# Kernel tuning notes

Hardware: AMD Instinct MI355X
Metric: run time of the kernel (lower is better)

## Reference

```python
import jax, jax.numpy as jnp
import numpy as np

N_NODES = 65536
N_EDGES = 1048576
IN_DIM = 128
OUT_DIM = 64


def setup_inputs() -> dict:
    key = jax.random.key(0)
    k = jax.random.split(key, 7)
    stdv = 1.0 / np.sqrt(OUT_DIM)
    return {
        "input_feature": jax.random.normal(k[0], (N_NODES, IN_DIM), dtype=jnp.float32),
        "edge_row": jax.random.randint(k[1], (N_EDGES,), 0, N_NODES, dtype=jnp.int32),
        "edge_col": jax.random.randint(k[2], (N_EDGES,), 0, N_NODES, dtype=jnp.int32),
        "edge_vals": jax.random.uniform(k[3], (N_EDGES,), dtype=jnp.float32),
        "prior_probability_tensor": jax.random.uniform(k[4], (N_NODES, OUT_DIM), dtype=jnp.float32),
        "weight": jax.random.uniform(k[5], (IN_DIM, OUT_DIM), minval=-stdv, maxval=stdv, dtype=jnp.float32),
        "bias": jax.random.uniform(k[6], (OUT_DIM,), minval=-stdv, maxval=stdv, dtype=jnp.float32),
    }


def reference(input_feature, edge_row, edge_col, edge_vals, prior_probability_tensor, weight, bias):
    # support = X @ W  : [N, out_dim]
    support = input_feature @ weight
    # sparse spmm: out[i] = sum_e A[i, col(e)] * support[col(e)] over edges with row(e)==i
    msgs = edge_vals[:, None] * support[edge_col]          # [E, out_dim] gather
    output = jax.ops.segment_sum(msgs, edge_row, num_segments=input_feature.shape[0])
    # gate branch fires since output_dim == prior dim; then bias add
    return prior_probability_tensor * output + bias
```

## Files before the change

### kernel.cpp

```cpp
#include <hip/hip_runtime.h>
#include <hip/hip_fp16.h>

#define N_NODES 65536
#define N_EDGES 1048576
#define IN_DIM 128
#define OUT_DIM 64
#define NBUCK 1024
#define BROWS 64
#define EPB 4096
#define SLABC 1280
#define GEMM_BLOCKS (N_NODES / 64)
#define STAGE_BLOCKS (N_EDGES / EPB)

typedef __attribute__((ext_vector_type(8))) short short8;
typedef __attribute__((ext_vector_type(4))) float f32x4;

__device__ __forceinline__ short bf16b(float x) {
    union { float f; unsigned int u; } c; c.f = x;
    unsigned int r = (c.u + 0x7FFFu + ((c.u >> 16) & 1u)) >> 16;
    return (short)r;
}

__global__ __launch_bounds__(256) void gemm_stage_kernel(const float* __restrict__ X,
                                                         const float* __restrict__ W,
                                                         __half* __restrict__ S,
                                                         const int* __restrict__ erow,
                                                         const int* __restrict__ ecol,
                                                         const float* __restrict__ evals,
                                                         int* __restrict__ gcur,
                                                         uint2* __restrict__ staged) {
    if (blockIdx.x < GEMM_BLOCKS) {
        const int wid = threadIdx.x >> 6;
        const int lane = threadIdx.x & 63;
        const int row0 = blockIdx.x * 64 + wid * 16;
        const int lrow = lane & 15;
        const int hi = lane >> 4;

        short8 bfr[4][4];
#pragma unroll
        for (int ct = 0; ct < 4; ++ct) {
            const float* wp = W + (size_t)(hi * 8) * OUT_DIM + ct * 16 + lrow;
#pragma unroll
            for (int kt = 0; kt < 4; ++kt) {
                const float* wk = wp + (size_t)kt * 32 * OUT_DIM;
#pragma unroll
                for (int j = 0; j < 8; ++j)
                    bfr[ct][kt][j] = bf16b(wk[(size_t)j * OUT_DIM]);
            }
        }

        f32x4 acc[4] = {};
#pragma unroll
        for (int kt = 0; kt < 4; ++kt) {
            const float* xp = X + (size_t)(row0 + lrow) * IN_DIM + kt * 32 + hi * 8;
            float4 x0 = *reinterpret_cast<const float4*>(xp);
            float4 x1 = *reinterpret_cast<const float4*>(xp + 4);
            short8 af;
            af[0] = bf16b(x0.x); af[1] = bf16b(x0.y); af[2] = bf16b(x0.z); af[3] = bf16b(x0.w);
            af[4] = bf16b(x1.x); af[5] = bf16b(x1.y); af[6] = bf16b(x1.z); af[7] = bf16b(x1.w);
#pragma unroll
            for (int ct = 0; ct < 4; ++ct)
                acc[ct] = __builtin_amdgcn_mfma_f32_16x16x32_bf16(af, bfr[ct][kt], acc[ct], 0, 0, 0);
        }
#pragma unroll
        for (int ct = 0; ct < 4; ++ct)
#pragma unroll
            for (int r = 0; r < 4; ++r)
                S[(size_t)(row0 + hi * 4 + r) * OUT_DIM + ct * 16 + lrow] =
                    __float2half_rn(acc[ct][r]);
    } else {
        __shared__ int cnt[NBUCK];
        __shared__ int base[NBUCK];
        __shared__ int cnt2[NBUCK];
        const int t = threadIdx.x;
        for (int i = t; i < NBUCK; i += 256) { cnt[i] = 0; cnt2[i] = 0; }
        __syncthreads();

        unsigned int rc[16];
        float v[16];
        const int e0 = (blockIdx.x - GEMM_BLOCKS) * EPB;
#pragma unroll
        for (int i = 0; i < 16; ++i) {
            int e = e0 + i * 256 + t;
            unsigned int r = (unsigned int)erow[e];
            unsigned int c = (unsigned int)ecol[e];
            rc[i] = (r << 16) | c;
            v[i] = evals[e];
            atomicAdd(&cnt[r >> 6], 1);
        }
        __syncthreads();
        for (int i = t; i < NBUCK; i += 256) {
            int c = cnt[i];
            if (c) base[i] = i * SLABC + atomicAdd(&gcur[i], c);
        }
        __syncthreads();
#pragma unroll
        for (int i = 0; i < 16; ++i) {
            int b = rc[i] >> 22;
            int pos = base[b] + atomicAdd(&cnt2[b], 1);
            if (pos < (b + 1) * SLABC)
                staged[pos] = make_uint2(rc[i], __float_as_uint(v[i]));
        }
    }
}

__device__ __forceinline__ int wave_incl_scan(int v, int lane) {
#pragma unroll
    for (int d = 1; d < 64; d <<= 1) {
        int t = __shfl_up(v, d, 64);
        if (lane >= d) v += t;
    }
    return v;
}

__global__ __launch_bounds__(512) void sort_gather_kernel(const int* __restrict__ gcur,
                                                          const uint2* __restrict__ slab,
                                                          const __half* __restrict__ S,
                                                          const float* __restrict__ prior,
                                                          const float* __restrict__ bias,
                                                          float* __restrict__ out) {
    __shared__ uint2 scvp[SLABC];
    __shared__ int cnt[BROWS];
    __shared__ int excl[BROWS];
    __shared__ int cnt2[BROWS];
    const int t = threadIdx.x;
    const int b = blockIdx.x;
    const int count = min(gcur[b], SLABC);
    const uint2* ms = slab + (size_t)b * SLABC;

    if (t < BROWS) { cnt[t] = 0; cnt2[t] = 0; }
    __syncthreads();

    uint2 ent[3];
    unsigned int lr[3];
#pragma unroll
    for (int i = 0; i < 3; ++i) {
        int idx = i * 512 + t;
        if (idx < count) {
            ent[i] = ms[idx];
            lr[i] = (ent[i].x >> 16) & (BROWS - 1);
            atomicAdd(&cnt[lr[i]], 1);
        }
    }
    __syncthreads();
    if (t < 64) {
        int v = cnt[t];
        int inc = wave_incl_scan(v, t);
        excl[t] = inc - v;
    }
    __syncthreads();
#pragma unroll
    for (int i = 0; i < 3; ++i) {
        int idx = i * 512 + t;
        if (idx < count) {
            int pos = excl[lr[i]] + atomicAdd(&cnt2[lr[i]], 1);
            scvp[pos] = ent[i];
        }
    }
    __syncthreads();

    const int g = t >> 4;
    const int sub = t & 15;
    const ushort4* S4 = reinterpret_cast<const ushort4*>(S);
#pragma unroll
    for (int nn = 0; nn < 2; ++nn) {
        const int lrow = g * 2 + nn;
        const int start = excl[lrow];
        const int end = start + cnt[lrow];
        float ax = 0.f, ay = 0.f, az = 0.f, aw = 0.f;
        for (int j = start; j < end; j += 8) {
            uint2 e[8];
            float w[8];
#pragma unroll
            for (int q = 0; q < 8; ++q) {
                int idx = j + q;
                bool valid = idx < end;
                e[q] = scvp[valid ? idx : start];
                w[q] = valid ? __uint_as_float(e[q].y) : 0.f;
            }
            ushort4 s[8];
#pragma unroll
            for (int q = 0; q < 8; ++q)
                s[q] = S4[(size_t)(e[q].x & 0xFFFFu) * 16 + sub];
#pragma unroll
            for (int q = 0; q < 8; ++q) {
                ax += w[q] * __half2float(__ushort_as_half(s[q].x));
                ay += w[q] * __half2float(__ushort_as_half(s[q].y));
                az += w[q] * __half2float(__ushort_as_half(s[q].z));
                aw += w[q] * __half2float(__ushort_as_half(s[q].w));
            }
        }
        const size_t nbase = (size_t)(b * BROWS + lrow) * OUT_DIM + sub * 4;
        f32x4 p = __builtin_nontemporal_load(reinterpret_cast<const f32x4*>(prior + nbase));
        float4 bb = *reinterpret_cast<const float4*>(&bias[sub * 4]);
        f32x4 r;
        r.x = p.x * ax + bb.x;
        r.y = p.y * ay + bb.y;
        r.z = p.z * az + bb.z;
        r.w = p.w * aw + bb.w;
        __builtin_nontemporal_store(r, reinterpret_cast<f32x4*>(out + nbase));
    }
}

extern "C" void kernel_launch(void* const* d_in, const int* in_sizes, int n_in,
                              void* d_out, int out_size, void* d_ws, size_t ws_size,
                              hipStream_t stream) {
    const float* X     = (const float*)d_in[0];
    const int*   erow  = (const int*)d_in[1];
    const int*   ecol  = (const int*)d_in[2];
    const float* evals = (const float*)d_in[3];
    const float* prior = (const float*)d_in[4];
    const float* W     = (const float*)d_in[5];
    const float* bias  = (const float*)d_in[6];
    float* out = (float*)d_out;

    char* ws = (char*)d_ws;
    __half* S    = (__half*)ws;
    uint2*  slab = (uint2*)(ws + 8388608);
    int*    gcur = (int*)(ws + 8388608 + 10485760);

    hipMemsetAsync(gcur, 0, NBUCK * sizeof(int), stream);
    gemm_stage_kernel<<<GEMM_BLOCKS + STAGE_BLOCKS, 256, 0, stream>>>(
        X, W, S, erow, ecol, evals, gcur, slab);
    sort_gather_kernel<<<NBUCK, 512, 0, stream>>>(gcur, slab, S, prior, bias, out);
}
```

Baseline: 57.03 us.

## Split support matrix into two column halves and gather in two passes

```diff
diff --git a/kernel.cpp b/kernel.cpp
--- a/kernel.cpp
+++ b/kernel.cpp
@@ -14,6 +14,8 @@
 
 typedef __attribute__((ext_vector_type(8))) short short8;
 typedef __attribute__((ext_vector_type(4))) float f32x4;
+typedef __attribute__((ext_vector_type(2))) float f32x2;
+typedef __attribute__((ext_vector_type(2))) unsigned int u32x2;
 
 __device__ __forceinline__ short bf16b(float x) {
     union { float f; unsigned int u; } c; c.f = x;
@@ -23,7 +25,8 @@
 
 __global__ __launch_bounds__(256) void gemm_stage_kernel(const float* __restrict__ X,
                                                          const float* __restrict__ W,
-                                                         __half* __restrict__ S,
+                                                         __half* __restrict__ S_lo,
+                                                         __half* __restrict__ S_hi,
                                                          const int* __restrict__ erow,
                                                          const int* __restrict__ ecol,
                                                          const float* __restrict__ evals,
@@ -63,11 +66,13 @@
                 acc[ct] = __builtin_amdgcn_mfma_f32_16x16x32_bf16(af, bfr[ct][kt], acc[ct], 0, 0, 0);
         }
 #pragma unroll
-        for (int ct = 0; ct < 4; ++ct)
+        for (int ct = 0; ct < 4; ++ct) {
+            __half* Sp = (ct < 2) ? S_lo : S_hi;
+            const int cip = (ct & 1) * 16 + lrow;
 #pragma unroll
             for (int r = 0; r < 4; ++r)
-                S[(size_t)(row0 + hi * 4 + r) * OUT_DIM + ct * 16 + lrow] =
-                    __float2half_rn(acc[ct][r]);
+                Sp[(size_t)(row0 + hi * 4 + r) * 32 + cip] = __float2half_rn(acc[ct][r]);
+        }
     } else {
         __shared__ int cnt[NBUCK];
         __shared__ int base[NBUCK];
@@ -115,7 +120,8 @@
 
 __global__ __launch_bounds__(512) void sort_gather_kernel(const int* __restrict__ gcur,
                                                           const uint2* __restrict__ slab,
-                                                          const __half* __restrict__ S,
+                                                          const __half* __restrict__ S_lo,
+                                                          const __half* __restrict__ S_hi,
                                                           const float* __restrict__ prior,
                                                           const float* __restrict__ bias,
                                                           float* __restrict__ out) {
@@ -126,18 +132,18 @@
     const int t = threadIdx.x;
     const int b = blockIdx.x;
     const int count = min(gcur[b], SLABC);
-    const uint2* ms = slab + (size_t)b * SLABC;
+    const u32x2* ms = reinterpret_cast<const u32x2*>(slab + (size_t)b * SLABC);
 
     if (t < BROWS) { cnt[t] = 0; cnt2[t] = 0; }
     __syncthreads();
 
-    uint2 ent[3];
+    u32x2 ent[3];
     unsigned int lr[3];
 #pragma unroll
     for (int i = 0; i < 3; ++i) {
         int idx = i * 512 + t;
         if (idx < count) {
-            ent[i] = ms[idx];
+            ent[i] = __builtin_nontemporal_load(&ms[idx]);
             lr[i] = (ent[i].x >> 16) & (BROWS - 1);
             atomicAdd(&cnt[lr[i]], 1);
         }
@@ -154,51 +160,52 @@
         int idx = i * 512 + t;
         if (idx < count) {
             int pos = excl[lr[i]] + atomicAdd(&cnt2[lr[i]], 1);
-            scvp[pos] = ent[i];
+            scvp[pos] = make_uint2(ent[i].x, ent[i].y);
         }
     }
     __syncthreads();
 
     const int g = t >> 4;
     const int sub = t & 15;
-    const ushort4* S4 = reinterpret_cast<const ushort4*>(S);
-#pragma unroll
-    for (int nn = 0; nn < 2; ++nn) {
-        const int lrow = g * 2 + nn;
-        const int start = excl[lrow];
-        const int end = start + cnt[lrow];
-        float ax = 0.f, ay = 0.f, az = 0.f, aw = 0.f;
-        for (int j = start; j < end; j += 8) {
-            uint2 e[8];
-            float w[8];
-#pragma unroll
-            for (int q = 0; q < 8; ++q) {
-                int idx = j + q;
-                bool valid = idx < end;
-                e[q] = scvp[valid ? idx : start];
-                w[q] = valid ? __uint_as_float(e[q].y) : 0.f;
+#pragma unroll
+    for (int pass = 0; pass < 2; ++pass) {
+        const ushort2* Sp = reinterpret_cast<const ushort2*>(pass ? S_hi : S_lo);
+#pragma unroll
+        for (int nn = 0; nn < 2; ++nn) {
+            const int lrow = g * 2 + nn;
+            const int start = excl[lrow];
+            const int end = start + cnt[lrow];
+            float ax = 0.f, ay = 0.f;
+            for (int j = start; j < end; j += 8) {
+                unsigned int col[8];
+                float w[8];
+#pragma unroll
+                for (int q = 0; q < 8; ++q) {
+                    int idx = j + q;
+                    bool valid = idx < end;
+                    uint2 e = scvp[valid ? idx : start];
+                    col[q] = e.x & 0xFFFFu;
+                    w[q] = valid ? __uint_as_float(e.y) : 0.f;
+                }
+                ushort2 s[8];
+#pragma unroll
+                for (int q = 0; q < 8; ++q)
+                    s[q] = Sp[(size_t)col[q] * 16 + sub];
+#pragma unroll
+                for (int q = 0; q < 8; ++q) {
+                    ax += w[q] * __half2float(__ushort_as_half(s[q].x));
+                    ay += w[q] * __half2float(__ushort_as_half(s[q].y));
+                }
             }
-            ushort4 s[8];
-#pragma unroll
-            for (int q = 0; q < 8; ++q)
-                s[q] = S4[(size_t)(e[q].x & 0xFFFFu) * 16 + sub];
-#pragma unroll
-            for (int q = 0; q < 8; ++q) {
-                ax += w[q] * __half2float(__ushort_as_half(s[q].x));
-                ay += w[q] * __half2float(__ushort_as_half(s[q].y));
-                az += w[q] * __half2float(__ushort_as_half(s[q].z));
-                aw += w[q] * __half2float(__ushort_as_half(s[q].w));
-            }
-        }
-        const size_t nbase = (size_t)(b * BROWS + lrow) * OUT_DIM + sub * 4;
-        f32x4 p = __builtin_nontemporal_load(reinterpret_cast<const f32x4*>(prior + nbase));
-        float4 bb = *reinterpret_cast<const float4*>(&bias[sub * 4]);
-        f32x4 r;
-        r.x = p.x * ax + bb.x;
-        r.y = p.y * ay + bb.y;
-        r.z = p.z * az + bb.z;
-        r.w = p.w * aw + bb.w;
-        __builtin_nontemporal_store(r, reinterpret_cast<f32x4*>(out + nbase));
+            const size_t nbase = (size_t)(b * BROWS + lrow) * OUT_DIM + pass * 32 + sub * 2;
+            f32x2 p = __builtin_nontemporal_load(reinterpret_cast<const f32x2*>(prior + nbase));
+            const float bx = bias[pass * 32 + sub * 2];
+            const float by = bias[pass * 32 + sub * 2 + 1];
+            f32x2 r;
+            r.x = p.x * ax + bx;
+            r.y = p.y * ay + by;
+            __builtin_nontemporal_store(r, reinterpret_cast<f32x2*>(out + nbase));
+        }
     }
 }
 
@@ -215,12 +222,13 @@
     float* out = (float*)d_out;
 
     char* ws = (char*)d_ws;
-    __half* S    = (__half*)ws;
+    __half* S_lo = (__half*)ws;
+    __half* S_hi = (__half*)(ws + 4194304);
     uint2*  slab = (uint2*)(ws + 8388608);
     int*    gcur = (int*)(ws + 8388608 + 10485760);
 
     hipMemsetAsync(gcur, 0, NBUCK * sizeof(int), stream);
     gemm_stage_kernel<<<GEMM_BLOCKS + STAGE_BLOCKS, 256, 0, stream>>>(
-        X, W, S, erow, ecol, evals, gcur, slab);
-    sort_gather_kernel<<<NBUCK, 512, 0, stream>>>(gcur, slab, S, prior, bias, out);
-}
+        X, W, S_lo, S_hi, erow, ecol, evals, gcur, slab);
+    sort_gather_kernel<<<NBUCK, 512, 0, stream>>>(gcur, slab, S_lo, S_hi, prior, bias, out);
+}
```

Result: slower. 63.24 us (+10.9%).
